# Performance work log

Measured on AMD Instinct MI355X. Metric: run time of the kernel, lower is better.

## Reference

```python
import jax, jax.numpy as jnp
import numpy as np

D_IN, D_OUT, K = 128, 256, 16
B, N = 2, 16384
D_HALF = D_OUT // 2
EPS = 1e-6
GROUPS = 16


def conv1x1(x, w, b):
    # x: (B,C,N,K), w: (O,C), b: (O,)
    return jnp.einsum('oc,bcnk->bonk', w, x) + b[None, :, None, None]


def groupnorm(x, w, b, groups=GROUPS):
    Bv, C, Nv, Kv = x.shape
    xr = x.reshape(Bv, groups, C // groups, Nv, Kv)
    m = xr.mean(axis=(2, 3, 4), keepdims=True)
    v = xr.var(axis=(2, 3, 4), keepdims=True)
    xn = ((xr - m) / jnp.sqrt(v + EPS)).reshape(Bv, C, Nv, Kv)
    return xn * w[None, :, None, None] + b[None, :, None, None]


def lse(coords, x, idx, dist, w, b, gw, gb):
    # coords: (B,N,3); x: (B,C,N,1); idx: (B,N,K); dist: (B,N,K)
    nbr = jax.vmap(lambda c, i: c[i])(coords, idx)          # (B,N,K,3)
    ctr = jnp.broadcast_to(coords[:, :, None, :], nbr.shape)  # (B,N,K,3)
    rel = jnp.concatenate([ctr, nbr, ctr - nbr], axis=-1)    # (B,N,K,9)
    geo = jnp.concatenate([rel.transpose(0, 3, 1, 2), dist[:, None, :, :]], axis=1)  # (B,10,N,K)
    geo = jax.nn.relu(groupnorm(conv1x1(geo, w, b), gw, gb))  # (B,d/2,N,K)
    nf = jax.vmap(lambda f, i: f[:, i])(x[..., 0], idx)       # (B,d/2,N,K)
    return jnp.concatenate([geo, nf], axis=1)                 # (B,d,N,K)


def attentive_pool(x, w, b, gw, gb):
    m = x.mean(axis=-1, keepdims=True)  # (B,C,N,1)
    return jax.nn.relu(groupnorm(conv1x1(m, w, b), gw, gb))


def setup_inputs() -> dict:
    key = jax.random.key(0)
    ks = jax.random.split(key, 16)
    s = 0.02
    d = {
        'coords': jax.random.normal(ks[0], (B, N, 3), jnp.float32),
        'features': jax.random.normal(ks[1], (B, D_IN, N, 1), jnp.float32),
        'knn_dist': jax.random.uniform(ks[2], (B, N, K), jnp.float32),
        'knn_idx': jax.random.randint(ks[3], (B, N, K), 0, N),
        'w1': jax.random.normal(ks[4], (D_HALF, D_IN), jnp.float32) * s,
        'b1': jnp.zeros((D_HALF,), jnp.float32),
        'lse1_w': jax.random.normal(ks[5], (D_HALF, 10), jnp.float32) * s,
        'lse1_b': jnp.zeros((D_HALF,), jnp.float32),
        'lse1_gw': jnp.ones((D_HALF,), jnp.float32),
        'lse1_gb': jnp.zeros((D_HALF,), jnp.float32),
        'pool1_w': jax.random.normal(ks[6], (D_HALF, D_OUT), jnp.float32) * s,
        'pool1_b': jnp.zeros((D_HALF,), jnp.float32),
        'pool1_gw': jnp.ones((D_HALF,), jnp.float32),
        'pool1_gb': jnp.zeros((D_HALF,), jnp.float32),
        'lse2_w': jax.random.normal(ks[7], (D_HALF, 10), jnp.float32) * s,
        'lse2_b': jnp.zeros((D_HALF,), jnp.float32),
        'lse2_gw': jnp.ones((D_HALF,), jnp.float32),
        'lse2_gb': jnp.zeros((D_HALF,), jnp.float32),
        'pool2_w': jax.random.normal(ks[8], (D_OUT, D_OUT), jnp.float32) * s,
        'pool2_b': jnp.zeros((D_OUT,), jnp.float32),
        'pool2_gw': jnp.ones((D_OUT,), jnp.float32),
        'pool2_gb': jnp.zeros((D_OUT,), jnp.float32),
        'mlp2_w': jax.random.normal(ks[9], (2 * D_OUT, D_OUT), jnp.float32) * s,
        'mlp2_b': jnp.zeros((2 * D_OUT,), jnp.float32),
        'sc_w': jax.random.normal(ks[10], (2 * D_OUT, D_IN), jnp.float32) * s,
        'sc_b': jnp.zeros((2 * D_OUT,), jnp.float32),
        'sc_gw': jnp.ones((2 * D_OUT,), jnp.float32),
        'sc_gb': jnp.zeros((2 * D_OUT,), jnp.float32),
    }
    return d


def reference(coords, features, knn_dist, knn_idx,
              w1, b1,
              lse1_w, lse1_b, lse1_gw, lse1_gb,
              pool1_w, pool1_b, pool1_gw, pool1_gb,
              lse2_w, lse2_b, lse2_gw, lse2_gb,
              pool2_w, pool2_b, pool2_gw, pool2_gb,
              mlp2_w, mlp2_b, sc_w, sc_b, sc_gw, sc_gb):
    # mlp1: conv + LeakyReLU(0.2), no norm
    x = jax.nn.leaky_relu(conv1x1(features, w1, b1), 0.2)        # (B,d/2,N,1)
    x = lse(coords, x, knn_idx, knn_dist, lse1_w, lse1_b, lse1_gw, lse1_gb)  # (B,d,N,K)
    x = attentive_pool(x, pool1_w, pool1_b, pool1_gw, pool1_gb)  # (B,d/2,N,1)
    x = lse(coords, x, knn_idx, knn_dist, lse2_w, lse2_b, lse2_gw, lse2_gb)  # (B,d,N,K)
    x = attentive_pool(x, pool2_w, pool2_b, pool2_gw, pool2_gb)  # (B,d,N,1)
    main = conv1x1(x, mlp2_w, mlp2_b)                            # (B,2d,N,1)
    short = groupnorm(conv1x1(features, sc_w, sc_b), sc_gw, sc_gb)
    return jax.nn.leaky_relu(main + short, 0.01)                 # (B,2d,N,1)
```

## Files before the change

### kernel.cpp

```cpp
#include <hip/hip_runtime.h>


constexpr int Bc = 2;
constexpr int Nc = 16384;
constexpr int Kc = 16;
constexpr float EPSc = 1e-6f;

typedef __attribute__((ext_vector_type(8))) short short8;
typedef __attribute__((ext_vector_type(4))) short short4v;
typedef __attribute__((ext_vector_type(4))) float floatx4;

__device__ inline short f2bf(float x) {
    union { float f; unsigned u; } v; v.f = x;
    unsigned r = v.u + 0x7fffu + ((v.u >> 16) & 1u);
    return (short)(r >> 16);
}
__device__ inline float bf2f(short s) {
    union { unsigned u; float f; } v;
    v.u = ((unsigned)(unsigned short)s) << 16;
    return v.f;
}

constexpr size_t OW_P1W = 0;
constexpr size_t OW_P2W = OW_P1W + 128*256;
constexpr size_t OW_M2W = OW_P2W + 256*256;
constexpr size_t OW_SCW = OW_M2W + 512*256;
constexpr size_t OW_W1  = OW_SCW + 512*128;
constexpr size_t OW_L1W = OW_W1  + 128*128;
constexpr size_t OW_L2W = OW_L1W + 128*32;
constexpr size_t OW_FB  = OW_L2W + 128*32;
constexpr size_t OW_X1  = OW_FB  + (size_t)Bc*Nc*128;
constexpr size_t OW_M   = OW_X1  + (size_t)Bc*Nc*128;
constexpr size_t OW_Z1  = OW_M   + (size_t)Bc*Nc*256;
constexpr size_t OW_Z2  = OW_Z1  + (size_t)Bc*Nc*128;
constexpr size_t OW_S   = OW_Z2  + (size_t)Bc*Nc*256;

constexpr int CV0 = 128*256;
constexpr int CV1 = CV0 + 256*256;
constexpr int CV2 = CV1 + 512*256;
constexpr int CV3 = CV2 + 512*128;
constexpr int CV4 = CV3 + 128*128;
constexpr int CV5 = CV4 + 128*32;
constexpr int CV6 = CV5 + 128*32;
constexpr int CVTOT = CV6 + 512;

__global__ void prep_kernel(const float* __restrict__ p1w,
                            const float* __restrict__ p2w,
                            const float* __restrict__ m2w,
                            const float* __restrict__ scw,
                            const float* __restrict__ w1,
                            const float* __restrict__ l1w,
                            const float* __restrict__ l2w,
                            short* __restrict__ W16,
                            float* __restrict__ ST)
{
    int i = blockIdx.x * 256 + threadIdx.x;
    if (i < CV0) { W16[OW_P1W + i] = f2bf(p1w[i]); return; }
    if (i < CV1) { int k = i - CV0; W16[OW_P2W + k] = f2bf(p2w[k]); return; }
    if (i < CV2) { int k = i - CV1; W16[OW_M2W + k] = f2bf(m2w[k]); return; }
    if (i < CV3) { int k = i - CV2; W16[OW_SCW + k] = f2bf(scw[k]); return; }
    if (i < CV4) { int k = i - CV3; W16[OW_W1  + k] = f2bf(w1[k]); return; }
    if (i < CV5) { int k = i - CV4; int o = k >> 5, c = k & 31;
                   W16[OW_L1W + k] = (c < 10) ? f2bf(l1w[o*10+c]) : (short)0; return; }
    if (i < CV6) { int k = i - CV5; int o = k >> 5, c = k & 31;
                   W16[OW_L2W + k] = (c < 10) ? f2bf(l2w[o*10+c]) : (short)0; return; }
    { int k = i - CV6; if (k < 512) ST[k] = 0.f; }
}

__global__ void feat_t_kernel(const float* __restrict__ in, short* __restrict__ out) {
    int tid  = threadIdx.x;
    int lane = tid & 63, wave = tid >> 6;
    int bb = blockIdx.x / (Nc / 64);
    int n  = (blockIdx.x % (Nc / 64)) * 64 + lane;
    #pragma unroll
    for (int cc = 0; cc < 4; cc++) {
        int c0 = (wave + cc * 4) * 8;
        short8 sv;
        #pragma unroll
        for (int i = 0; i < 8; i++)
            sv[i] = f2bf(in[((size_t)bb * 128 + c0 + i) * Nc + n]);
        *(short8*)&out[((size_t)(bb * Nc + n)) * 128 + c0] = sv;
    }
}

__launch_bounds__(256)
__global__ void geo_reduce_kernel(const float* __restrict__ coords,
                                  const int* __restrict__ knn_idx,
                                  const float* __restrict__ knn_dist,
                                  float* __restrict__ dst)
{
    __shared__ float part[4][65];
    const int tid  = threadIdx.x;
    const int b    = blockIdx.y;
    const int base = blockIdx.x * 256 + tid;
    const float* cb  = coords   + (size_t)b * Nc * 3;
    const int*   ib  = knn_idx  + (size_t)b * Nc * Kc;
    const float* db  = knn_dist + (size_t)b * Nc * Kc;

    float acc[65];
    #pragma unroll
    for (int i = 0; i < 65; i++) acc[i] = 0.f;

    #pragma unroll
    for (int it = 0; it < 4; it++) {
        int r = base + it * 65536;
        int n = r >> 4;
        float cx = cb[n*3+0], cy = cb[n*3+1], cz = cb[n*3+2];
        int   j  = ib[r];
        float nx = cb[j*3+0], ny = cb[j*3+1], nz = cb[j*3+2];
        float d  = db[r];
        float g[10] = {cx,cy,cz,nx,ny,nz,cx-nx,cy-ny,cz-nz,d};
        #pragma unroll
        for (int c = 0; c < 10; c++) acc[c] += g[c];
        int idx = 10;
        #pragma unroll
        for (int c = 0; c < 10; c++)
            #pragma unroll
            for (int c2 = c; c2 < 10; c2++) acc[idx++] += g[c] * g[c2];
    }
    #pragma unroll
    for (int i = 0; i < 65; i++) {
        float v = acc[i];
        #pragma unroll
        for (int off = 1; off < 64; off <<= 1) v += __shfl_xor(v, off);
        acc[i] = v;
    }
    int lane = tid & 63, wave = tid >> 6;
    if (lane == 0) {
        #pragma unroll
        for (int i = 0; i < 65; i++) part[wave][i] = acc[i];
    }
    __syncthreads();
    if (tid < 65) {
        float s = part[0][tid] + part[1][tid] + part[2][tid] + part[3][tid];
        atomicAdd(&dst[b * 65 + tid], s);
    }
}

__launch_bounds__(512)
__global__ void lse_param_kernel(const float* __restrict__ geoS,
                                 const float* __restrict__ l1w,
                                 const float* __restrict__ l1b,
                                 const float* __restrict__ l1gw,
                                 const float* __restrict__ l1gb,
                                 const float* __restrict__ l2w,
                                 const float* __restrict__ l2b,
                                 const float* __restrict__ l2gw,
                                 const float* __restrict__ l2gb,
                                 float* __restrict__ lp)
{
    __shared__ float osum[512], osq[512];
    const int tid = threadIdx.x;
    const int s = tid >> 8, r = tid & 255, b = r >> 7, o = r & 127;
    const float* wf = s ? l2w : l1w;
    const float* bf = s ? l2b : l1b;
    const float* gwf = s ? l2gw : l1gw;
    const float* gbf = s ? l2gb : l1gb;
    const float NK = (float)(Nc * Kc);
    const float* S = geoS + b * 65;

    float w[10];
    #pragma unroll
    for (int c = 0; c < 10; c++) w[c] = wf[o * 10 + c];
    float wS = 0.f;
    #pragma unroll
    for (int c = 0; c < 10; c++) wS += w[c] * S[c];
    float q = 0.f;
    {
        int idx = 10;
        #pragma unroll
        for (int c = 0; c < 10; c++)
            #pragma unroll
            for (int c2 = c; c2 < 10; c2++) {
                float t = w[c] * w[c2] * S[idx++];
                q += (c == c2) ? t : 2.f * t;
            }
    }
    float bo = bf[o];
    osum[tid] = NK * bo + wS;
    osq[tid]  = NK * bo * bo + 2.f * bo * wS + q;
    __syncthreads();
    int gb0 = tid & ~7;
    float gs = 0.f, gq = 0.f;
    #pragma unroll
    for (int i = 0; i < 8; i++) { gs += osum[gb0 + i]; gq += osq[gb0 + i]; }
    float cnt  = 8.f * NK;
    float mean = gs / cnt;
    float var  = gq / cnt - mean * mean;
    float iv   = rsqrtf(var + EPSc);
    float psc  = iv * gwf[o];
    float psh  = (bo - mean) * psc + gbf[o];
    lp[s * 512 + b * 256 + o]       = psc;
    lp[s * 512 + b * 256 + 128 + o] = psh;
}

template<int CIN, int COUT, int GROUP_CH, int MODE>
__launch_bounds__(256)
__global__ void gemm_conv(const short* __restrict__ wA,
                          const short* __restrict__ xB,
                          const float* __restrict__ bias,
                          short* __restrict__ outb,
                          float* __restrict__ outf,
                          float* __restrict__ stats,
                          const short* __restrict__ sbuf,
                          const float* __restrict__ st_sc,
                          const float* __restrict__ gw,
                          const float* __restrict__ gb,
                          float sc_cnt,
                          const float* __restrict__ bst,
                          const float* __restrict__ bgw,
                          const float* __restrict__ bgb,
                          float bcnt,
                          const float* __restrict__ bias2,
                          short* __restrict__ outb2)
{
    __shared__ short Abuf[128 * 40];
    __shared__ short Bbuf[128 * 40];
    __shared__ float sstat[32];
    __shared__ float smean[4], sinv[4];
    __shared__ float bsc[256], bsh[256];

    const int tid  = threadIdx.x;
    const int n0   = blockIdx.x * 128;
    const int mo   = blockIdx.y * 128;
    const int b    = blockIdx.z;
    const int lane = tid & 63;
    const int wave = tid >> 6;
    const int wm   = (wave >> 1) * 64;
    const int wn   = (wave & 1) * 64;
    const int l15  = lane & 15;
    const int quad = lane >> 4;
    const bool sc_tile = (MODE == 4) && (mo < 512);

    if constexpr (MODE == 2 || MODE == 4) { if (tid < 32) sstat[tid] = 0.f; }
    if constexpr (MODE == 3) {
        if (tid < 4) {
            int g = (mo >> 5) + tid;
            float s0 = st_sc[(b * 16 + g) * 2 + 0];
            float s1 = st_sc[(b * 16 + g) * 2 + 1];
            float mean = s0 / sc_cnt;
            float var  = s1 / sc_cnt - mean * mean;
            smean[tid] = mean;
            sinv[tid]  = rsqrtf(var + EPSc);
        }
        if (tid < CIN) {
            int g = tid >> 4;
            float s0 = bst[(b * 16 + g) * 2 + 0];
            float s1 = bst[(b * 16 + g) * 2 + 1];
            float mean = s0 / bcnt;
            float var  = s1 / bcnt - mean * mean;
            float inv  = rsqrtf(var + EPSc);
            float sc_  = inv * bgw[tid];
            bsc[tid] = sc_;
            bsh[tid] = bgb[tid] - mean * sc_;
        }
    }

    floatx4 acc[4][4];
    #pragma unroll
    for (int mi = 0; mi < 4; mi++)
        #pragma unroll
        for (int ni = 0; ni < 4; ni++)
            acc[mi][ni] = (floatx4){0.f, 0.f, 0.f, 0.f};

    const short* wAr = wA + (size_t)mo * CIN;
    const short* xBr = xB + (size_t)b * Nc * CIN + (size_t)n0 * CIN;

    for (int c0 = 0; c0 < CIN; c0 += 32) {
        __syncthreads();
        #pragma unroll
        for (int s = 0; s < 2; s++) {
            int e = tid + s * 256;
            int r = e >> 2, q = e & 3;
            *(short8*)&Abuf[r * 40 + q * 8] =
                *(const short8*)(wAr + (size_t)r * CIN + c0 + q * 8);
            short8 v = *(const short8*)(xBr + (size_t)r * CIN + c0 + q * 8);
            if constexpr (MODE == 3) {
                #pragma unroll
                for (int i = 0; i < 8; i++) {
                    int ch = c0 + q * 8 + i;
                    float t = bf2f(v[i]) * bsc[ch] + bsh[ch];
                    v[i] = f2bf(t > 0.f ? t : 0.f);
                }
            }
            *(short8*)&Bbuf[r * 40 + q * 8] = v;
        }
        __syncthreads();

        short8 af[4], bfr[4];
        #pragma unroll
        for (int mi = 0; mi < 4; mi++)
            af[mi] = *(short8*)&Abuf[(wm + mi * 16 + l15) * 40 + quad * 8];
        #pragma unroll
        for (int ni = 0; ni < 4; ni++)
            bfr[ni] = *(short8*)&Bbuf[(wn + ni * 16 + l15) * 40 + quad * 8];
        #pragma unroll
        for (int mi = 0; mi < 4; mi++)
            #pragma unroll
            for (int ni = 0; ni < 4; ni++)
                acc[mi][ni] = __builtin_amdgcn_mfma_f32_16x16x32_bf16(
                    af[mi], bfr[ni], acc[mi][ni], 0, 0, 0);
    }

    #pragma unroll
    for (int mi = 0; mi < 4; mi++) {
        int rowl = wm + mi * 16 + quad * 4;
        float b4[4], gw4[4], gb4[4];
        #pragma unroll
        for (int r = 0; r < 4; r++) {
            if constexpr (MODE == 4) {
                b4[r] = sc_tile ? bias[mo + rowl + r] : bias2[mo - 512 + rowl + r];
            } else {
                b4[r] = bias[mo + rowl + r];
            }
            if constexpr (MODE == 3) {
                gw4[r] = gw[mo + rowl + r];
                gb4[r] = gb[mo + rowl + r];
            }
        }
        float gs = 0.f, gq = 0.f;
        #pragma unroll
        for (int ni = 0; ni < 4; ni++) {
            int col = n0 + wn + ni * 16 + l15;
            if constexpr (MODE == 3) {
                short4v s4 = *(const short4v*)&sbuf[((size_t)(b * Nc + col)) * 512 + mo + rowl];
                int gl = rowl >> 5;
                #pragma unroll
                for (int r = 0; r < 4; r++) {
                    float v = acc[mi][ni][r] + b4[r];
                    float s = bf2f(s4[r]);
                    float sn = (s - smean[gl]) * sinv[gl] * gw4[r] + gb4[r];
                    float o = v + sn;
                    o = o > 0.f ? o : 0.01f * o;
                    outf[((size_t)b * COUT + mo + rowl + r) * Nc + col] = o;
                }
            } else if constexpr (MODE == 4) {
                short4v sv;
                #pragma unroll
                for (int r = 0; r < 4; r++) {
                    float v = acc[mi][ni][r] + b4[r];
                    if (sc_tile) { gs += v; gq += v * v; }
                    else v = v > 0.f ? v : 0.2f * v;
                    sv[r] = f2bf(v);
                }
                if (sc_tile)
                    *(short4v*)&outb[((size_t)(b * Nc + col)) * 512 + mo + rowl] = sv;
                else
                    *(short4v*)&outb2[((size_t)(b * Nc + col)) * 128 + mo - 512 + rowl] = sv;
            } else {
                short4v sv;
                #pragma unroll
                for (int r = 0; r < 4; r++) {
                    float v = acc[mi][ni][r] + b4[r];
                    if constexpr (MODE == 1) v = v > 0.f ? v : 0.2f * v;
                    if constexpr (MODE == 2) { gs += v; gq += v * v; }
                    sv[r] = f2bf(v);
                }
                *(short4v*)&outb[((size_t)(b * Nc + col)) * COUT + mo + rowl] = sv;
            }
        }
        if ((MODE == 2) || (MODE == 4 && sc_tile)) {
            #pragma unroll
            for (int off = 1; off < 16; off <<= 1) {
                gs += __shfl_xor(gs, off);
                gq += __shfl_xor(gq, off);
            }
            if (l15 == 0) {
                int gl = rowl / GROUP_CH;
                atomicAdd(&sstat[gl * 2 + 0], gs);
                atomicAdd(&sstat[gl * 2 + 1], gq);
            }
        }
    }
    if ((MODE == 2) || (MODE == 4 && sc_tile)) {
        __syncthreads();
        constexpr int NG = 128 / GROUP_CH;
        if (tid < 2 * NG) {
            int g0 = mo / GROUP_CH;
            atomicAdd(&stats[b * 32 + (g0 + (tid >> 1)) * 2 + (tid & 1)], sstat[tid]);
        }
    }
}

__launch_bounds__(256)
__global__ void lse_m_kernel(const float* __restrict__ coords,
                             const int* __restrict__ knn_idx,
                             const float* __restrict__ knn_dist,
                             const short* __restrict__ xprev,
                             const short* __restrict__ wpad,
                             const float* __restrict__ lp,
                             const float* __restrict__ xst,
                             const float* __restrict__ xgw,
                             const float* __restrict__ xgb,
                             float xcnt,
                             short* __restrict__ m)
{
    __shared__ short Bbuf[256 * 40];
    __shared__ int   jl[256];
    __shared__ float xscs[128], xshs[128];

    const int tid = threadIdx.x;
    const int b   = blockIdx.x >> 10;
    const int n0  = (blockIdx.x & 1023) * 16;
    const bool norm = (xst != nullptr);

    if (norm && tid < 128) {
        int g = tid >> 3;
        float s0 = xst[(b * 16 + g) * 2 + 0];
        float s1 = xst[(b * 16 + g) * 2 + 1];
        float mean = s0 / xcnt;
        float var  = s1 / xcnt - mean * mean;
        float inv  = rsqrtf(var + EPSc);
        float sc_  = inv * xgw[tid];
        xscs[tid] = sc_;
        xshs[tid] = xgb[tid] - mean * sc_;
    }
    {
        int pt = tid & 15, k = tid >> 4;
        int n  = n0 + pt;
        const float* cb = coords + (size_t)b * Nc * 3;
        float cx = cb[n*3+0], cy = cb[n*3+1], cz = cb[n*3+2];
        int   j  = knn_idx[((size_t)b * Nc + n) * Kc + k];
        float nx = cb[j*3+0], ny = cb[j*3+1], nz = cb[j*3+2];
        float d  = knn_dist[((size_t)b * Nc + n) * Kc + k];
        int col = k * 16 + pt;
        short8 w0, w1, zz;
        w0[0]=f2bf(cx); w0[1]=f2bf(cy); w0[2]=f2bf(cz);
        w0[3]=f2bf(nx); w0[4]=f2bf(ny); w0[5]=f2bf(nz);
        w0[6]=f2bf(cx-nx); w0[7]=f2bf(cy-ny);
        w1[0]=f2bf(cz-nz); w1[1]=f2bf(d);
        #pragma unroll
        for (int i = 2; i < 8; i++) w1[i] = 0;
        #pragma unroll
        for (int i = 0; i < 8; i++) zz[i] = 0;
        *(short8*)&Bbuf[col * 40 + 0]  = w0;
        *(short8*)&Bbuf[col * 40 + 8]  = w1;
        *(short8*)&Bbuf[col * 40 + 16] = zz;
        *(short8*)&Bbuf[col * 40 + 24] = zz;
        jl[col] = j;
    }
    __syncthreads();

    const int lane = tid & 63, wave = tid >> 6;
    const int l15 = lane & 15, quad = lane >> 4;
    short8 bfr[16];
    #pragma unroll
    for (int ni = 0; ni < 16; ni++)
        bfr[ni] = *(short8*)&Bbuf[(ni * 16 + l15) * 40 + quad * 8];
    #pragma unroll
    for (int mt2 = 0; mt2 < 2; mt2++) {
        int mt = wave * 2 + mt2;
        short8 af = *(const short8*)(wpad + (mt * 16 + l15) * 32 + quad * 8);
        floatx4 acc[16];
        #pragma unroll
        for (int ni = 0; ni < 16; ni++) {
            acc[ni] = (floatx4){0.f, 0.f, 0.f, 0.f};
            acc[ni] = __builtin_amdgcn_mfma_f32_16x16x32_bf16(af, bfr[ni], acc[ni], 0, 0, 0);
        }
        short4v sv;
        #pragma unroll
        for (int r = 0; r < 4; r++) {
            int o = mt * 16 + quad * 4 + r;
            float psc = lp[b * 256 + o];
            float psh = lp[b * 256 + 128 + o];
            float s = 0.f;
            #pragma unroll
            for (int ni = 0; ni < 16; ni++) {
                float v = acc[ni][r] * psc + psh;
                s += v > 0.f ? v : 0.f;
            }
            sv[r] = f2bf(s * (1.f / 16.f));
        }
        *(short4v*)&m[((size_t)(b * Nc + n0 + l15)) * 256 + mt * 16 + quad * 4] = sv;
    }

    {
        int tp = tid & 15, cs = tid >> 4;
        float sc8[8], sh8[8];
        if (norm) {
            #pragma unroll
            for (int i = 0; i < 8; i++) { sc8[i] = xscs[cs*8+i]; sh8[i] = xshs[cs*8+i]; }
        }
        float acc8[8];
        #pragma unroll
        for (int i = 0; i < 8; i++) acc8[i] = 0.f;
        #pragma unroll
        for (int k = 0; k < 16; k++) {
            int j = jl[k * 16 + tp];
            short8 v = *(const short8*)&xprev[((size_t)(b * Nc + j)) * 128 + cs * 8];
            if (norm) {
                #pragma unroll
                for (int i = 0; i < 8; i++) {
                    float t = bf2f(v[i]) * sc8[i] + sh8[i];
                    acc8[i] += t > 0.f ? t : 0.f;
                }
            } else {
                #pragma unroll
                for (int i = 0; i < 8; i++) acc8[i] += bf2f(v[i]);
            }
        }
        short8 sv;
        #pragma unroll
        for (int i = 0; i < 8; i++) sv[i] = f2bf(acc8[i] * (1.f / 16.f));
        *(short8*)&m[((size_t)(b * Nc + n0 + tp)) * 256 + 128 + cs * 8] = sv;
    }
}

extern "C" void kernel_launch(void* const* d_in, const int* in_sizes, int n_in,
                              void* d_out, int out_size, void* d_ws, size_t ws_size,
                              hipStream_t stream)
{
    const float* coords   = (const float*)d_in[0];
    const float* features = (const float*)d_in[1];
    const float* knn_dist = (const float*)d_in[2];
    const int*   knn_idx  = (const int*)  d_in[3];
    const float* w1       = (const float*)d_in[4];
    const float* b1       = (const float*)d_in[5];
    const float* lse1_w   = (const float*)d_in[6];
    const float* lse1_b   = (const float*)d_in[7];
    const float* lse1_gw  = (const float*)d_in[8];
    const float* lse1_gb  = (const float*)d_in[9];
    const float* pool1_w  = (const float*)d_in[10];
    const float* pool1_b  = (const float*)d_in[11];
    const float* pool1_gw = (const float*)d_in[12];
    const float* pool1_gb = (const float*)d_in[13];
    const float* lse2_w   = (const float*)d_in[14];
    const float* lse2_b   = (const float*)d_in[15];
    const float* lse2_gw  = (const float*)d_in[16];
    const float* lse2_gb  = (const float*)d_in[17];
    const float* pool2_w  = (const float*)d_in[18];
    const float* pool2_b  = (const float*)d_in[19];
    const float* pool2_gw = (const float*)d_in[20];
    const float* pool2_gb = (const float*)d_in[21];
    const float* mlp2_w   = (const float*)d_in[22];
    const float* mlp2_b   = (const float*)d_in[23];
    const float* sc_w     = (const float*)d_in[24];
    const float* sc_b     = (const float*)d_in[25];
    const float* sc_gw    = (const float*)d_in[26];
    const float* sc_gb    = (const float*)d_in[27];
    (void)in_sizes; (void)n_in; (void)out_size; (void)ws_size;

    float* ST = (float*)d_ws;
    float* ST_SC  = ST + 0;
    float* ST_P1  = ST + 64;
    float* ST_P2  = ST + 128;
    float* ST_GEO = ST + 256;
    float* ST_LP  = ST + 512;
    short* W16 = (short*)(ST + 2048);
    short* P1Wb = W16 + OW_P1W;
    short* P2Wb = W16 + OW_P2W;
    short* M2Wb = W16 + OW_M2W;
    short* SCWb = W16 + OW_SCW;
    short* L1Wb = W16 + OW_L1W;
    short* L2Wb = W16 + OW_L2W;
    short* FB   = W16 + OW_FB;
    short* X1B  = W16 + OW_X1;
    short* MB   = W16 + OW_M;
    short* Z1   = W16 + OW_Z1;
    short* Z2   = W16 + OW_Z2;
    short* SB   = W16 + OW_S;
    float* out  = (float*)d_out;

    prep_kernel<<<(CVTOT + 255) / 256, 256, 0, stream>>>(
        pool1_w, pool2_w, mlp2_w, sc_w, w1, lse1_w, lse2_w, W16, ST);
    feat_t_kernel<<<Bc * Nc / 64, 256, 0, stream>>>(features, FB);
    geo_reduce_kernel<<<dim3(256, Bc), 256, 0, stream>>>(
        coords, knn_idx, knn_dist, ST_GEO);
    lse_param_kernel<<<1, 512, 0, stream>>>(
        ST_GEO, lse1_w, lse1_b, lse1_gw, lse1_gb,
        lse2_w, lse2_b, lse2_gw, lse2_gb, ST_LP);

    gemm_conv<128,640,32,4><<<dim3(Nc/128, 5, Bc), 256, 0, stream>>>(
        SCWb, FB, sc_b, SB, nullptr, ST_SC, nullptr, nullptr, nullptr, nullptr, 0.f,
        nullptr, nullptr, nullptr, 0.f, b1, X1B);
    lse_m_kernel<<<Bc * Nc / 16, 256, 0, stream>>>(
        coords, knn_idx, knn_dist, X1B, L1Wb, ST_LP,
        nullptr, nullptr, nullptr, 0.f, MB);
    gemm_conv<256,128,8,2><<<dim3(Nc/128, 1, Bc), 256, 0, stream>>>(
        P1Wb, MB, pool1_b, Z1, nullptr, ST_P1, nullptr, nullptr, nullptr, nullptr, 0.f,
        nullptr, nullptr, nullptr, 0.f, nullptr, nullptr);
    lse_m_kernel<<<Bc * Nc / 16, 256, 0, stream>>>(
        coords, knn_idx, knn_dist, Z1, L2Wb, ST_LP + 512,
        ST_P1, pool1_gw, pool1_gb, (float)(8 * Nc), MB);
    gemm_conv<256,256,16,2><<<dim3(Nc/128, 2, Bc), 256, 0, stream>>>(
        P2Wb, MB, pool2_b, Z2, nullptr, ST_P2, nullptr, nullptr, nullptr, nullptr, 0.f,
        nullptr, nullptr, nullptr, 0.f, nullptr, nullptr);
    gemm_conv<256,512,32,3><<<dim3(Nc/128, 4, Bc), 256, 0, stream>>>(
        M2Wb, Z2, mlp2_b, nullptr, out, nullptr, SB, ST_SC, sc_gw, sc_gb,
        (float)(32 * Nc), ST_P2, pool2_gw, pool2_gb, (float)(16 * Nc),
        nullptr, nullptr);
}
```

Baseline: 335.4 us.

## Prefetch neighbor gathers before MFMA and cut register pressure in lse_m_kernel

The gathered neighbor-feature loads are now issued at the start of lse_m_kernel, before the MFMA section, so their global-memory latency can overlap with the matrix work. B fragments are read from LDS two at a time instead of all 16 being held in registers, and the scale/shift values are loaded as vectors up front. Together with __launch_bounds__(256, 4), this aims to fit more waves per CU. The gather thread mapping is also swapped so 16 consecutive threads read one contiguous 256-byte row, for better coalescing. The risk is that 16 live gather vectors raise register pressure again, which could cause spills under the new launch bound.

```diff
diff --git a/kernel.cpp b/kernel.cpp
--- a/kernel.cpp
+++ b/kernel.cpp
@@ -382,7 +382,7 @@
     }
 }
 
-__launch_bounds__(256)
+__launch_bounds__(256, 4)
 __global__ void lse_m_kernel(const float* __restrict__ coords,
                              const int* __restrict__ knn_idx,
                              const float* __restrict__ knn_dist,
@@ -442,40 +442,52 @@
     __syncthreads();
 
     const int lane = tid & 63, wave = tid >> 6;
-    const int l15 = lane & 15, quad = lane >> 4;
-    short8 bfr[16];
-    #pragma unroll
-    for (int ni = 0; ni < 16; ni++)
-        bfr[ni] = *(short8*)&Bbuf[(ni * 16 + l15) * 40 + quad * 8];
+    const int l15 = lane & 63 & 15, quad = (tid & 63) >> 4;
+
+    short8 af0 = *(const short8*)(wpad + ((wave * 2 + 0) * 16 + l15) * 32 + quad * 8);
+    short8 af1 = *(const short8*)(wpad + ((wave * 2 + 1) * 16 + l15) * 32 + quad * 8);
+    floatx4 psc0 = *(const floatx4*)&lp[b * 256 + (wave * 2 + 0) * 16 + quad * 4];
+    floatx4 psh0 = *(const floatx4*)&lp[b * 256 + 128 + (wave * 2 + 0) * 16 + quad * 4];
+    floatx4 psc1 = *(const floatx4*)&lp[b * 256 + (wave * 2 + 1) * 16 + quad * 4];
+    floatx4 psh1 = *(const floatx4*)&lp[b * 256 + 128 + (wave * 2 + 1) * 16 + quad * 4];
+
+    const int tp = tid >> 4, cs = tid & 15;
+    short8 gv[16];
+    #pragma unroll
+    for (int k = 0; k < 16; k++) {
+        int j = jl[k * 16 + tp];
+        gv[k] = *(const short8*)&xprev[((size_t)(b * Nc + j)) * 128 + cs * 8];
+    }
+
     #pragma unroll
     for (int mt2 = 0; mt2 < 2; mt2++) {
-        int mt = wave * 2 + mt2;
-        short8 af = *(const short8*)(wpad + (mt * 16 + l15) * 32 + quad * 8);
-        floatx4 acc[16];
-        #pragma unroll
-        for (int ni = 0; ni < 16; ni++) {
-            acc[ni] = (floatx4){0.f, 0.f, 0.f, 0.f};
-            acc[ni] = __builtin_amdgcn_mfma_f32_16x16x32_bf16(af, bfr[ni], acc[ni], 0, 0, 0);
+        const int mt = wave * 2 + mt2;
+        const short8 af = mt2 ? af1 : af0;
+        const floatx4 psc4 = mt2 ? psc1 : psc0;
+        const floatx4 psh4 = mt2 ? psh1 : psh0;
+        float s4[4] = {0.f, 0.f, 0.f, 0.f};
+        #pragma unroll
+        for (int nb = 0; nb < 8; nb++) {
+            short8 f0 = *(short8*)&Bbuf[((nb * 2 + 0) * 16 + l15) * 40 + quad * 8];
+            short8 f1 = *(short8*)&Bbuf[((nb * 2 + 1) * 16 + l15) * 40 + quad * 8];
+            floatx4 a0 = __builtin_amdgcn_mfma_f32_16x16x32_bf16(
+                af, f0, (floatx4){0.f, 0.f, 0.f, 0.f}, 0, 0, 0);
+            floatx4 a1 = __builtin_amdgcn_mfma_f32_16x16x32_bf16(
+                af, f1, (floatx4){0.f, 0.f, 0.f, 0.f}, 0, 0, 0);
+            #pragma unroll
+            for (int r = 0; r < 4; r++) {
+                float v0 = a0[r] * psc4[r] + psh4[r];
+                float v1 = a1[r] * psc4[r] + psh4[r];
+                s4[r] += (v0 > 0.f ? v0 : 0.f) + (v1 > 0.f ? v1 : 0.f);
+            }
         }
         short4v sv;
         #pragma unroll
-        for (int r = 0; r < 4; r++) {
-            int o = mt * 16 + quad * 4 + r;
-            float psc = lp[b * 256 + o];
-            float psh = lp[b * 256 + 128 + o];
-            float s = 0.f;
-            #pragma unroll
-            for (int ni = 0; ni < 16; ni++) {
-                float v = acc[ni][r] * psc + psh;
-                s += v > 0.f ? v : 0.f;
-            }
-            sv[r] = f2bf(s * (1.f / 16.f));
-        }
+        for (int r = 0; r < 4; r++) sv[r] = f2bf(s4[r] * (1.f / 16.f));
         *(short4v*)&m[((size_t)(b * Nc + n0 + l15)) * 256 + mt * 16 + quad * 4] = sv;
     }
 
     {
-        int tp = tid & 15, cs = tid >> 4;
         float sc8[8], sh8[8];
         if (norm) {
             #pragma unroll
@@ -484,19 +496,20 @@
         float acc8[8];
         #pragma unroll
         for (int i = 0; i < 8; i++) acc8[i] = 0.f;
-        #pragma unroll
-        for (int k = 0; k < 16; k++) {
-            int j = jl[k * 16 + tp];
-            short8 v = *(const short8*)&xprev[((size_t)(b * Nc + j)) * 128 + cs * 8];
-            if (norm) {
+        if (norm) {
+            #pragma unroll
+            for (int k = 0; k < 16; k++) {
                 #pragma unroll
                 for (int i = 0; i < 8; i++) {
-                    float t = bf2f(v[i]) * sc8[i] + sh8[i];
+                    float t = bf2f(gv[k][i]) * sc8[i] + sh8[i];
                     acc8[i] += t > 0.f ? t : 0.f;
                 }
-            } else {
+            }
+        } else {
+            #pragma unroll
+            for (int k = 0; k < 16; k++) {
                 #pragma unroll
-                for (int i = 0; i < 8; i++) acc8[i] += bf2f(v[i]);
+                for (int i = 0; i < 8; i++) acc8[i] += bf2f(gv[k][i]);
             }
         }
         short8 sv;
```

Result: slower. 566.5 us (+68.9%).
